# Performance work log

Hardware: AMD Instinct MI355X
Metric: run time of the kernel (lower is better)

## Reference

```python
import jax, jax.numpy as jnp
import numpy as np

E = 1024
H = 16
CH = E // H

def setup_inputs() -> dict:
    key = jax.random.key(0)
    ks = jax.random.split(key, 9)
    s = E ** -0.5
    return {
        'x': jax.random.normal(ks[0], (4, 2048, E), dtype=jnp.float32),
        'Wq': jax.random.normal(ks[1], (E, E), dtype=jnp.float32) * s,
        'bq': jnp.zeros((E,), dtype=jnp.float32),
        'Wk': jax.random.normal(ks[2], (E, E), dtype=jnp.float32) * s,
        'bk': jnp.zeros((E,), dtype=jnp.float32),
        'Wv': jax.random.normal(ks[3], (E, E), dtype=jnp.float32) * s,
        'bv': jnp.zeros((E,), dtype=jnp.float32),
        'Wo': jax.random.normal(ks[4], (E, E), dtype=jnp.float32) * s,
        'bo': jnp.zeros((E,), dtype=jnp.float32),
    }

def _split_heads(t):
    # [..., n, H*ch] -> [..., H, n, ch]
    b, n, e = t.shape
    return t.reshape(b, n, H, CH).transpose(0, 2, 1, 3)

def reference(x, Wq, bq, Wk, bk, Wv, bv, Wo, bo):
    scale = CH ** -0.5
    q = _split_heads(x @ Wq.T + bq)  # [b,H,n,ch]
    k = _split_heads(x @ Wk.T + bk)
    v = _split_heads(x @ Wv.T + bv)
    att = jnp.einsum('bhqc,bhkc->bhqk', q, k) * scale
    att = jax.nn.softmax(att, axis=-1)
    out = jnp.einsum('bhqk,bhkc->bhqc', att, v)  # [b,H,n,ch]
    b, h, n, c = out.shape
    out = out.transpose(0, 2, 1, 3).reshape(b, n, h * c)
    return out @ Wo.T + bo
```

## Files before the change

### kernel.cpp

```cpp
#include <hip/hip_runtime.h>
#include <stdint.h>

#define EMB   1024
#define NHEAD 16
#define CHD   64
#define NB    4
#define SEQ   2048
#define NTOK  (NB * SEQ)
#define KDIM  1024

typedef __attribute__((ext_vector_type(8))) short  bf16x8;
typedef __attribute__((ext_vector_type(4))) short  short4v;
typedef __attribute__((ext_vector_type(4))) float  f32x4;
typedef __attribute__((ext_vector_type(4))) float  float4v;

__device__ __forceinline__ short f2bf(float f) {
    unsigned int u = __float_as_uint(f);
    u += 0x7fffu + ((u >> 16) & 1u);
    return (short)(u >> 16);
}

__device__ __forceinline__ void async16(const short* g, short* l) {
    __builtin_amdgcn_global_load_lds((__attribute__((address_space(1))) void const*)g,
                                     (__attribute__((address_space(3))) void*)l, 16, 0, 0);
}

__global__ __launch_bounds__(256) void cvt_all(const float* __restrict__ x,
                                               const float* __restrict__ Wq,
                                               const float* __restrict__ Wk,
                                               const float* __restrict__ Wv,
                                               const float* __restrict__ Wo,
                                               short* __restrict__ xb,
                                               short* __restrict__ Wqb,
                                               short* __restrict__ Wkb,
                                               short* __restrict__ Wvb,
                                               short* __restrict__ Wob) {
    int bid = blockIdx.x;
    const float* src;
    short* dst;
    int idx;
    if (bid < 8192) {
        src = x; dst = xb; idx = bid * 256 + threadIdx.x;
    } else {
        int w  = (bid - 8192) >> 10;
        int lb = (bid - 8192) & 1023;
        src = (w == 0) ? Wq : (w == 1) ? Wk : (w == 2) ? Wv : Wo;
        dst = (w == 0) ? Wqb : (w == 1) ? Wkb : (w == 2) ? Wvb : Wob;
        idx = lb * 256 + threadIdx.x;
    }
    float4v v = ((const float4v*)src)[idx];
    short4v s;
    s.x = f2bf(v.x); s.y = f2bf(v.y); s.z = f2bf(v.z); s.w = f2bf(v.w);
    ((short4v*)dst)[idx] = s;
}

__device__ __forceinline__ void gemm_core(const short* __restrict__ Atile,
                                          const short* __restrict__ Btile,
                                          short* As, short* Bs, f32x4 acc[4][4]) {
    const int tid  = threadIdx.x;
    const int wave = tid >> 6, lane = tid & 63;
    const int quad = lane >> 4, l16 = lane & 15;
    const int wm = (wave >> 1) * 64, wn = (wave & 1) * 64;
    const int srow = lane >> 2;
    const int scol = (lane & 3) * 8;

    for (int k0 = 0; k0 < KDIM; k0 += 32) {
        __syncthreads();
#pragma unroll
        for (int c = 0; c < 2; ++c) {
            int chunk = wave * 2 + c;
            int row = chunk * 16 + srow;
            async16(Atile + (size_t)row * KDIM + k0 + scol, As + chunk * 512);
            async16(Btile + (size_t)row * KDIM + k0 + scol, Bs + chunk * 512);
        }
        __syncthreads();
        bf16x8 af[4], bfr[4];
#pragma unroll
        for (int i = 0; i < 4; ++i)
            af[i] = *(const bf16x8*)&As[(wm + i * 16 + l16) * 32 + quad * 8];
#pragma unroll
        for (int j = 0; j < 4; ++j)
            bfr[j] = *(const bf16x8*)&Bs[(wn + j * 16 + l16) * 32 + quad * 8];
#pragma unroll
        for (int i = 0; i < 4; ++i)
#pragma unroll
            for (int j = 0; j < 4; ++j)
                acc[i][j] = __builtin_amdgcn_mfma_f32_16x16x32_bf16(af[i], bfr[j], acc[i][j], 0, 0, 0);
    }
}

#define QSCALE 0.1803368801111204f
__global__ __launch_bounds__(256) void qkv_gemm(const short* __restrict__ xb,
                                                const short* __restrict__ Wqb,
                                                const short* __restrict__ Wkb,
                                                const short* __restrict__ Wvb,
                                                const float* __restrict__ bq,
                                                const float* __restrict__ bk,
                                                const float* __restrict__ bv,
                                                short* __restrict__ Qb,
                                                short* __restrict__ Kb,
                                                short* __restrict__ Vtb) {
    __shared__ short As[128 * 32], Bs[128 * 32];
    const int bm = blockIdx.x, bn = blockIdx.y;
    const int which = bn >> 3;
    const int ew = (bn & 7) * 128;
    const short* W    = (which == 0) ? Wqb : (which == 1) ? Wkb : Wvb;
    const float* bias = (which == 0) ? bq  : (which == 1) ? bk  : bv;
    const float sc    = (which == 0) ? QSCALE : 1.0f;

    const short* Xt = xb + (size_t)bm * 128 * KDIM;
    const short* Wt = W + (size_t)ew * KDIM;
    const short* Ap = (which == 2) ? Wt : Xt;
    const short* Bp = (which == 2) ? Xt : Wt;

    f32x4 acc[4][4];
    const f32x4 z = {0.f, 0.f, 0.f, 0.f};
#pragma unroll
    for (int i = 0; i < 4; ++i)
#pragma unroll
        for (int j = 0; j < 4; ++j) acc[i][j] = z;

    gemm_core(Ap, Bp, As, Bs, acc);

    const int lane = threadIdx.x & 63, wave = threadIdx.x >> 6;
    const int quad = lane >> 4, l16 = lane & 15;
    const int wm = (wave >> 1) * 64, wn = (wave & 1) * 64;

    if (which == 2) {
#pragma unroll
        for (int i = 0; i < 4; ++i)
#pragma unroll
            for (int j = 0; j < 4; ++j)
#pragma unroll
                for (int r = 0; r < 4; ++r) {
                    int e = ew + wm + i * 16 + quad * 4 + r;
                    int token = bm * 128 + wn + j * 16 + l16;
                    int bb = token >> 11, nn = token & 2047;
                    int hh = e >> 6, cc = e & 63;
                    Vtb[(((size_t)bb * NHEAD + hh) * CHD + cc) * SEQ + nn] =
                        f2bf(acc[i][j][r] + bias[e]);
                }
    } else {
        short* dst = which ? Kb : Qb;
#pragma unroll
        for (int i = 0; i < 4; ++i)
#pragma unroll
            for (int j = 0; j < 4; ++j)
#pragma unroll
                for (int r = 0; r < 4; ++r) {
                    int token = bm * 128 + wm + i * 16 + quad * 4 + r;
                    int bb = token >> 11, nn = token & 2047;
                    int e = ew + wn + j * 16 + l16;
                    int hh = e >> 6, cc = e & 63;
                    dst[(((size_t)bb * NHEAD + hh) * SEQ + nn) * CHD + cc] =
                        f2bf((acc[i][j][r] + bias[e]) * sc);
                }
    }
}

__global__ __launch_bounds__(256, 4) void attn(const short* __restrict__ Qb,
                                               const short* __restrict__ Kb,
                                               const short* __restrict__ Vtb,
                                               short* __restrict__ AOb) {
    __shared__ short Ks[16 * 512];
    __shared__ short Vs[16 * 512];

    const int qt = blockIdx.x;
    const int bh = blockIdx.y;
    const int tid = threadIdx.x, wave = tid >> 6, lane = tid & 63;
    const int quad = lane >> 4, l16 = lane & 15;

    const short* Kg = Kb  + (size_t)bh * SEQ * CHD;
    const short* Vg = Vtb + (size_t)bh * CHD * SEQ;

    const short* Qg = Qb + ((size_t)bh * SEQ + qt * 64 + wave * 16 + l16) * CHD;
    bf16x8 qf0 = *(const bf16x8*)(Qg + quad * 8);
    bf16x8 qf1 = *(const bf16x8*)(Qg + 32 + quad * 8);

    const int kr = lane >> 3, ku = (lane & 7) ^ kr;
    const int vr = lane >> 4, vu = (lane & 15) ^ (vr << 2);

    int koff[4], voff[4];
#pragma unroll
    for (int cc = 0; cc < 4; ++cc) {
        int c = wave * 4 + cc;
        int l = c * 8 + kr;
        int j = l >> 4, m = l & 15;
        int kvg = ((j >> 1) << 5) + ((m >> 2) << 3) + ((j & 1) << 2) + (m & 3);
        koff[cc] = kvg * CHD + ku * 8;
        voff[cc] = (c * 4 + vr) * SEQ + vu * 8;
    }

    const int krow = l16 & 7;
    const int kbase = ((l16 >> 3) * 512) + krow * 64;
    const short* kp0 = Ks + kbase + ((quad ^ krow) << 3);
    const short* kp1 = Ks + kbase + (((4 + quad) ^ krow) << 3);
    const int vrow = l16 & 3;
    const short* vp = Vs + (l16 >> 2) * 512 + vrow * 128 + quad * 8;

    const f32x4 zf = {0.f, 0.f, 0.f, 0.f};
    const bf16x8 onesv = {16256, 16256, 16256, 16256, 16256, 16256, 16256, 16256};
    f32x4 O[4];
#pragma unroll
    for (int nb = 0; nb < 4; ++nb) O[nb] = zf;
    f32x4 lacc = zf;

    const short* Kgp = Kg;
    const short* Vgp = Vg;

    for (int kt = 0; kt < 16; ++kt) {
        __syncthreads();
#pragma unroll
        for (int cc = 0; cc < 4; ++cc) {
            int c = wave * 4 + cc;
            async16(Kgp + koff[cc], Ks + c * 512);
            async16(Vgp + voff[cc], Vs + c * 512);
        }
        Kgp += 128 * CHD;
        Vgp += 128;
        __syncthreads();

        f32x4 sacc[8];
#pragma unroll
        for (int j = 0; j < 8; ++j) {
            bf16x8 k0 = *(const bf16x8*)(kp0 + j * 1024);
            bf16x8 k1 = *(const bf16x8*)(kp1 + j * 1024);
            f32x4 t = __builtin_amdgcn_mfma_f32_16x16x32_bf16(k0, qf0, zf, 0, 0, 0);
            sacc[j] = __builtin_amdgcn_mfma_f32_16x16x32_bf16(k1, qf1, t, 0, 0, 0);
        }

#pragma unroll
        for (int kk = 0; kk < 4; ++kk) {
            int d[4];
#pragma unroll
            for (int t = 0; t < 2; ++t) {
                f32x4 s4 = sacc[2 * kk + t];
                unsigned u0 = __float_as_uint(__builtin_amdgcn_exp2f(s4.x));
                unsigned u1 = __float_as_uint(__builtin_amdgcn_exp2f(s4.y));
                unsigned u2 = __float_as_uint(__builtin_amdgcn_exp2f(s4.z));
                unsigned u3 = __float_as_uint(__builtin_amdgcn_exp2f(s4.w));
                d[2 * t]     = __builtin_amdgcn_perm(u1, u0, 0x07060302u);
                d[2 * t + 1] = __builtin_amdgcn_perm(u3, u2, 0x07060302u);
            }
            union { int i[4]; bf16x8 v; } pf;
            pf.i[0] = d[0]; pf.i[1] = d[1]; pf.i[2] = d[2]; pf.i[3] = d[3];
            lacc = __builtin_amdgcn_mfma_f32_16x16x32_bf16(pf.v, onesv, lacc, 0, 0, 0);
            const short* vpk = vp + ((kk ^ vrow) << 5);
#pragma unroll
            for (int nb = 0; nb < 4; ++nb) {
                bf16x8 vf = *(const bf16x8*)(vpk + nb * 2048);
                O[nb] = __builtin_amdgcn_mfma_f32_16x16x32_bf16(pf.v, vf, O[nb], 0, 0, 0);
            }
        }
    }

    float linv[4];
#pragma unroll
    for (int r = 0; r < 4; ++r) linv[r] = 1.0f / lacc[r];

    const int b = bh >> 4, h = bh & 15;
#pragma unroll
    for (int nb = 0; nb < 4; ++nb)
#pragma unroll
        for (int r = 0; r < 4; ++r) {
            int n = qt * 64 + wave * 16 + quad * 4 + r;
            int cc = nb * 16 + l16;
            AOb[((size_t)b * SEQ + n) * EMB + h * CHD + cc] = f2bf(O[nb][r] * linv[r]);
        }
}

__global__ __launch_bounds__(256) void out_gemm(const short* __restrict__ AOb,
                                                const short* __restrict__ Wob,
                                                const float* __restrict__ bo,
                                                float* __restrict__ out) {
    __shared__ short As[128 * 32], Bs[128 * 32];
    const int bm = blockIdx.x, bn = blockIdx.y;

    f32x4 acc[4][4];
    const f32x4 z = {0.f, 0.f, 0.f, 0.f};
#pragma unroll
    for (int i = 0; i < 4; ++i)
#pragma unroll
        for (int j = 0; j < 4; ++j) acc[i][j] = z;

    gemm_core(AOb + (size_t)bm * 128 * KDIM, Wob + (size_t)bn * 128 * KDIM, As, Bs, acc);

    const int lane = threadIdx.x & 63, wave = threadIdx.x >> 6;
    const int quad = lane >> 4, l16 = lane & 15;
    const int wm = (wave >> 1) * 64, wn = (wave & 1) * 64;
#pragma unroll
    for (int i = 0; i < 4; ++i)
#pragma unroll
        for (int j = 0; j < 4; ++j)
#pragma unroll
            for (int r = 0; r < 4; ++r) {
                int token = bm * 128 + wm + i * 16 + quad * 4 + r;
                int e = bn * 128 + wn + j * 16 + l16;
                out[(size_t)token * EMB + e] = acc[i][j][r] + bo[e];
            }
}

extern "C" void kernel_launch(void* const* d_in, const int* in_sizes, int n_in,
                              void* d_out, int out_size, void* d_ws, size_t ws_size,
                              hipStream_t stream) {
    const float* x  = (const float*)d_in[0];
    const float* Wq = (const float*)d_in[1];
    const float* bq = (const float*)d_in[2];
    const float* Wk = (const float*)d_in[3];
    const float* bk = (const float*)d_in[4];
    const float* Wv = (const float*)d_in[5];
    const float* bv = (const float*)d_in[6];
    const float* Wo = (const float*)d_in[7];
    const float* bo = (const float*)d_in[8];

    char* ws = (char*)d_ws;
    short* xb  = (short*)(ws + 0);
    short* Wqb = (short*)(ws + (size_t)16 * 1024 * 1024);
    short* Wkb = (short*)(ws + (size_t)18 * 1024 * 1024);
    short* Wvb = (short*)(ws + (size_t)20 * 1024 * 1024);
    short* Wob = (short*)(ws + (size_t)22 * 1024 * 1024);
    short* Qb  = (short*)(ws + (size_t)24 * 1024 * 1024);
    short* Kb  = (short*)(ws + (size_t)40 * 1024 * 1024);
    short* Vtb = (short*)(ws + (size_t)56 * 1024 * 1024);
    short* AOb = (short*)(ws + (size_t)72 * 1024 * 1024);

    cvt_all<<<dim3(8192 + 4096), dim3(256), 0, stream>>>(x, Wq, Wk, Wv, Wo,
                                                         xb, Wqb, Wkb, Wvb, Wob);
    qkv_gemm<<<dim3(64, 24), dim3(256), 0, stream>>>(xb, Wqb, Wkb, Wvb, bq, bk, bv, Qb, Kb, Vtb);
    attn<<<dim3(32, 64), dim3(256), 0, stream>>>(Qb, Kb, Vtb, AOb);
    out_gemm<<<dim3(64, 8), dim3(256), 0, stream>>>(AOb, Wob, bo, (float*)d_out);
}
```

Before: 287.2 us.

## Process two 16-row query groups per wave in attention to reuse K/V fragments

Each wave in the attention kernel now handles 32 query rows (two 16-row groups) instead of 16, so one block covers 128 queries and the grid's query dimension is halved. K and V fragments read from LDS are reused across both query groups, halving LDS traffic and global K/V tile loads per query. The cost is more accumulator registers (two sets of O and row-sum accumulators) and half as many blocks, which may reduce occupancy.

```diff
diff --git a/kernel.cpp b/kernel.cpp
--- a/kernel.cpp
+++ b/kernel.cpp
@@ -173,9 +173,13 @@
     const short* Kg = Kb  + (size_t)bh * SEQ * CHD;
     const short* Vg = Vtb + (size_t)bh * CHD * SEQ;
 
-    const short* Qg = Qb + ((size_t)bh * SEQ + qt * 64 + wave * 16 + l16) * CHD;
-    bf16x8 qf0 = *(const bf16x8*)(Qg + quad * 8);
-    bf16x8 qf1 = *(const bf16x8*)(Qg + 32 + quad * 8);
+    bf16x8 qf0[2], qf1[2];
+#pragma unroll
+    for (int g = 0; g < 2; ++g) {
+        const short* Qg = Qb + ((size_t)bh * SEQ + qt * 128 + wave * 32 + g * 16 + l16) * CHD;
+        qf0[g] = *(const bf16x8*)(Qg + quad * 8);
+        qf1[g] = *(const bf16x8*)(Qg + 32 + quad * 8);
+    }
 
     const int kr = lane >> 3, ku = (lane & 7) ^ kr;
     const int vr = lane >> 4, vu = (lane & 15) ^ (vr << 2);
@@ -200,10 +204,13 @@
 
     const f32x4 zf = {0.f, 0.f, 0.f, 0.f};
     const bf16x8 onesv = {16256, 16256, 16256, 16256, 16256, 16256, 16256, 16256};
-    f32x4 O[4];
-#pragma unroll
-    for (int nb = 0; nb < 4; ++nb) O[nb] = zf;
-    f32x4 lacc = zf;
+    f32x4 O[2][4];
+#pragma unroll
+    for (int g = 0; g < 2; ++g)
+#pragma unroll
+        for (int nb = 0; nb < 4; ++nb) O[g][nb] = zf;
+    f32x4 lacc[2];
+    lacc[0] = zf; lacc[1] = zf;
 
     const short* Kgp = Kg;
     const short* Vgp = Vg;
@@ -220,53 +227,63 @@
         Vgp += 128;
         __syncthreads();
 
-        f32x4 sacc[8];
-#pragma unroll
-        for (int j = 0; j < 8; ++j) {
-            bf16x8 k0 = *(const bf16x8*)(kp0 + j * 1024);
-            bf16x8 k1 = *(const bf16x8*)(kp1 + j * 1024);
-            f32x4 t = __builtin_amdgcn_mfma_f32_16x16x32_bf16(k0, qf0, zf, 0, 0, 0);
-            sacc[j] = __builtin_amdgcn_mfma_f32_16x16x32_bf16(k1, qf1, t, 0, 0, 0);
-        }
-
 #pragma unroll
         for (int kk = 0; kk < 4; ++kk) {
-            int d[4];
-#pragma unroll
-            for (int t = 0; t < 2; ++t) {
-                f32x4 s4 = sacc[2 * kk + t];
-                unsigned u0 = __float_as_uint(__builtin_amdgcn_exp2f(s4.x));
-                unsigned u1 = __float_as_uint(__builtin_amdgcn_exp2f(s4.y));
-                unsigned u2 = __float_as_uint(__builtin_amdgcn_exp2f(s4.z));
-                unsigned u3 = __float_as_uint(__builtin_amdgcn_exp2f(s4.w));
-                d[2 * t]     = __builtin_amdgcn_perm(u1, u0, 0x07060302u);
-                d[2 * t + 1] = __builtin_amdgcn_perm(u3, u2, 0x07060302u);
+            bf16x8 kA0 = *(const bf16x8*)(kp0 + (2 * kk) * 1024);
+            bf16x8 kA1 = *(const bf16x8*)(kp1 + (2 * kk) * 1024);
+            bf16x8 kB0 = *(const bf16x8*)(kp0 + (2 * kk + 1) * 1024);
+            bf16x8 kB1 = *(const bf16x8*)(kp1 + (2 * kk + 1) * 1024);
+
+            union { int i[4]; bf16x8 v; } pf[2];
+#pragma unroll
+            for (int g = 0; g < 2; ++g) {
+                f32x4 sA = __builtin_amdgcn_mfma_f32_16x16x32_bf16(kA0, qf0[g], zf, 0, 0, 0);
+                sA = __builtin_amdgcn_mfma_f32_16x16x32_bf16(kA1, qf1[g], sA, 0, 0, 0);
+                f32x4 sB = __builtin_amdgcn_mfma_f32_16x16x32_bf16(kB0, qf0[g], zf, 0, 0, 0);
+                sB = __builtin_amdgcn_mfma_f32_16x16x32_bf16(kB1, qf1[g], sB, 0, 0, 0);
+
+                unsigned a0 = __float_as_uint(__builtin_amdgcn_exp2f(sA.x));
+                unsigned a1 = __float_as_uint(__builtin_amdgcn_exp2f(sA.y));
+                unsigned a2 = __float_as_uint(__builtin_amdgcn_exp2f(sA.z));
+                unsigned a3 = __float_as_uint(__builtin_amdgcn_exp2f(sA.w));
+                unsigned b0 = __float_as_uint(__builtin_amdgcn_exp2f(sB.x));
+                unsigned b1 = __float_as_uint(__builtin_amdgcn_exp2f(sB.y));
+                unsigned b2 = __float_as_uint(__builtin_amdgcn_exp2f(sB.z));
+                unsigned b3 = __float_as_uint(__builtin_amdgcn_exp2f(sB.w));
+                pf[g].i[0] = __builtin_amdgcn_perm(a1, a0, 0x07060302u);
+                pf[g].i[1] = __builtin_amdgcn_perm(a3, a2, 0x07060302u);
+                pf[g].i[2] = __builtin_amdgcn_perm(b1, b0, 0x07060302u);
+                pf[g].i[3] = __builtin_amdgcn_perm(b3, b2, 0x07060302u);
+
+                lacc[g] = __builtin_amdgcn_mfma_f32_16x16x32_bf16(pf[g].v, onesv, lacc[g], 0, 0, 0);
             }
-            union { int i[4]; bf16x8 v; } pf;
-            pf.i[0] = d[0]; pf.i[1] = d[1]; pf.i[2] = d[2]; pf.i[3] = d[3];
-            lacc = __builtin_amdgcn_mfma_f32_16x16x32_bf16(pf.v, onesv, lacc, 0, 0, 0);
+
             const short* vpk = vp + ((kk ^ vrow) << 5);
 #pragma unroll
             for (int nb = 0; nb < 4; ++nb) {
                 bf16x8 vf = *(const bf16x8*)(vpk + nb * 2048);
-                O[nb] = __builtin_amdgcn_mfma_f32_16x16x32_bf16(pf.v, vf, O[nb], 0, 0, 0);
+#pragma unroll
+                for (int g = 0; g < 2; ++g)
+                    O[g][nb] = __builtin_amdgcn_mfma_f32_16x16x32_bf16(pf[g].v, vf, O[g][nb], 0, 0, 0);
             }
         }
     }
 
-    float linv[4];
-#pragma unroll
-    for (int r = 0; r < 4; ++r) linv[r] = 1.0f / lacc[r];
-
     const int b = bh >> 4, h = bh & 15;
 #pragma unroll
-    for (int nb = 0; nb < 4; ++nb)
-#pragma unroll
-        for (int r = 0; r < 4; ++r) {
-            int n = qt * 64 + wave * 16 + quad * 4 + r;
-            int cc = nb * 16 + l16;
-            AOb[((size_t)b * SEQ + n) * EMB + h * CHD + cc] = f2bf(O[nb][r] * linv[r]);
-        }
+    for (int g = 0; g < 2; ++g) {
+        float linv[4];
+#pragma unroll
+        for (int r = 0; r < 4; ++r) linv[r] = 1.0f / lacc[g][r];
+#pragma unroll
+        for (int nb = 0; nb < 4; ++nb)
+#pragma unroll
+            for (int r = 0; r < 4; ++r) {
+                int n = qt * 128 + wave * 32 + g * 16 + quad * 4 + r;
+                int cc = nb * 16 + l16;
+                AOb[((size_t)b * SEQ + n) * EMB + h * CHD + cc] = f2bf(O[g][nb][r] * linv[r]);
+            }
+    }
 }
 
 __global__ __launch_bounds__(256) void out_gemm(const short* __restrict__ AOb,
@@ -327,6 +344,6 @@
     cvt_all<<<dim3(8192 + 4096), dim3(256), 0, stream>>>(x, Wq, Wk, Wv, Wo,
                                                          xb, Wqb, Wkb, Wvb, Wob);
     qkv_gemm<<<dim3(64, 24), dim3(256), 0, stream>>>(xb, Wqb, Wkb, Wvb, bq, bk, bv, Qb, Kb, Vtb);
-    attn<<<dim3(32, 64), dim3(256), 0, stream>>>(Qb, Kb, Vtb, AOb);
+    attn<<<dim3(16, 64), dim3(256), 0, stream>>>(Qb, Kb, Vtb, AOb);
     out_gemm<<<dim3(64, 8), dim3(256), 0, stream>>>(AOb, Wob, bo, (float*)d_out);
 }
```

New measurement: 281.8 us. No clear change (-1.9%).
